# Performance work log

Measured on AMD Instinct MI355X. Metric: run time of the kernel, lower is better.

The kernel has to match this reference:

```python
import jax, jax.numpy as jnp
import numpy as np
import math

B, N, M, D, HID, OUT = 8, 2048, 2048, 1024, 1024, 1024

def setup_inputs() -> dict:
    key = jax.random.key(0)
    k1, k2, k3, k4, k5, k6 = jax.random.split(key, 6)
    h1 = jax.random.normal(k1, (B, N, D), dtype=jnp.float32)
    h2 = jax.random.normal(k2, (B, M, D), dtype=jnp.float32)
    mask = jax.random.randint(k3, (B, N, M), 0, 2, dtype=jnp.int32)
    # nn.Linear(in, out, bias=False) weight has shape (out, in)
    Wq = jax.random.normal(k4, (HID, D), dtype=jnp.float32) / math.sqrt(D)
    Wk = jax.random.normal(k5, (HID, D), dtype=jnp.float32) / math.sqrt(D)
    Wv = jax.random.normal(k6, (OUT, D), dtype=jnp.float32) / math.sqrt(D)
    return {"h1": h1, "h2": h2, "mask": mask, "Wq": Wq, "Wk": Wk, "Wv": Wv}

def reference(h1, h2, mask, Wq, Wk, Wv):
    Q = jnp.einsum('bnd,hd->bnh', h1, Wq)            # (B,N,HID)
    K = jnp.einsum('bmd,hd->bmh', h2, Wk)            # (B,M,HID)
    V = jnp.einsum('bmd,od->bmo', h2, Wv)            # (B,M,OUT)
    E = jnp.einsum('bnh,bmh->bnm', Q, K)             # (B,N,M) scores
    # NOTE: original masks E BEFORE dividing by sqrt(hidden_d)
    E = jnp.where(mask == 0, jnp.float32(-1e10), E)
    A = jax.nn.softmax(E / math.sqrt(HID), axis=2)
    return jnp.einsum('bnm,bmo->bno', A, V)          # (B,N,OUT)
```

## Files before the change

kernel.cpp:

```cpp
#include <hip/hip_runtime.h>


using f16   = _Float16;
using f16x4 = __attribute__((ext_vector_type(4))) _Float16;
using f16x8 = __attribute__((ext_vector_type(8))) _Float16;
using f32x4 = __attribute__((ext_vector_type(4))) float;

typedef unsigned int u32_g __attribute__((address_space(1)));
typedef unsigned int u32_l __attribute__((address_space(3)));

__device__ __forceinline__ void gl_lds16(const f16* g, f16* l) {
    __builtin_amdgcn_global_load_lds((const u32_g*)g, (u32_l*)l, 16, 0, 0);
}

template <int EPI, int GDEC, int LGX>
__global__ __launch_bounds__(256)
void gemm_nt_f16(const f16* __restrict__ A, const f16* __restrict__ B,
                 void* __restrict__ Cv, const int* __restrict__ Mask,
                 int N, int K, long sA, long sB, long sC, long sMask)
{
    int bx, by, bz;
    if constexpr (GDEC == 0) {
        bx = blockIdx.x; by = blockIdx.y; bz = blockIdx.z;
    } else {
        int l = blockIdx.x;
        bz = l & 7; bx = (l >> 3) & ((1 << LGX) - 1); by = l >> (3 + LGX);
    }
    const f16* Ab = A + (long)bz * sA;
    const f16* Bb = B + (long)bz * sB;
    const int bm0 = by * 128;
    const int bn0 = bx * 128;

    const int tid  = threadIdx.x;
    const int lane = tid & 63;
    const int wid  = tid >> 6;
    const int wm   = (wid >> 1) * 64;
    const int wn   = (wid & 1)  * 64;
    const int lr   = lane & 15;
    const int quad = lane >> 4;

    __shared__ f16 As[128 * 32];
    __shared__ f16 Bs[128 * 32];

    const int r0 = tid >> 2, b0 = tid & 3;
    const int r1 = r0 + 64;
    const int k0blk = (b0 ^ ((r0 >> 1) & 3)) << 3;
    const int k1blk = (b0 ^ ((r1 >> 1) & 3)) << 3;
    const f16* gA0 = Ab + (long)(bm0 + r0) * K + k0blk;
    const f16* gA1 = Ab + (long)(bm0 + r1) * K + k1blk;
    const f16* gB0 = Bb + (long)(bn0 + r0) * K + k0blk;
    const f16* gB1 = Bb + (long)(bn0 + r1) * K + k1blk;
    f16* lA0 = As + wid * 512;
    f16* lA1 = As + 2048 + wid * 512;
    f16* lB0 = Bs + wid * 512;
    f16* lB1 = Bs + 2048 + wid * 512;

    const int kb = ((quad ^ ((lr >> 1) & 3)) << 3);

    f32x4 acc[4][4] = {};
    f32x4 rs[4] = {};
    f16x8 bones;
#pragma unroll
    for (int j = 0; j < 8; ++j) bones[j] = (f16)1.0f;

    for (int k0 = 0; k0 < K; k0 += 32) {
        gl_lds16(gA0 + k0, lA0);
        gl_lds16(gA1 + k0, lA1);
        gl_lds16(gB0 + k0, lB0);
        gl_lds16(gB1 + k0, lB1);
        __syncthreads();

        f16x8 af[4], bfr[4];
#pragma unroll
        for (int i = 0; i < 4; ++i)
            af[i] = *(const f16x8*)(&As[(wm + i * 16 + lr) * 32 + kb]);
#pragma unroll
        for (int j = 0; j < 4; ++j)
            bfr[j] = *(const f16x8*)(&Bs[(wn + j * 16 + lr) * 32 + kb]);

        if constexpr (EPI == 2) {
#pragma unroll
            for (int i = 0; i < 4; ++i)
                rs[i] = __builtin_amdgcn_mfma_f32_16x16x32_f16(af[i], bones, rs[i], 0, 0, 0);
        }
#pragma unroll
        for (int i = 0; i < 4; ++i)
#pragma unroll
            for (int j = 0; j < 4; ++j)
                acc[i][j] = __builtin_amdgcn_mfma_f32_16x16x32_f16(af[i], bfr[j], acc[i][j], 0, 0, 0);
        __syncthreads();
    }

    if constexpr (EPI == 0) {
        f16* C = (f16*)Cv + (long)bz * sC;
#pragma unroll
        for (int i = 0; i < 4; ++i)
#pragma unroll
            for (int j = 0; j < 4; ++j)
#pragma unroll
                for (int r = 0; r < 4; ++r) {
                    long idx = (long)(bm0 + wm + i * 16 + quad * 4 + r) * N
                             + (bn0 + wn + j * 16 + lr);
                    C[idx] = (f16)acc[i][j][r];
                }
    } else if constexpr (EPI == 1) {
        f16* C = (f16*)Cv + (long)bz * sC;
        const int* Mk = Mask + (long)bz * sMask;
#pragma unroll
        for (int i = 0; i < 4; ++i)
#pragma unroll
            for (int j = 0; j < 4; ++j)
#pragma unroll
                for (int r = 0; r < 4; ++r) {
                    long idx = (long)(bm0 + wm + i * 16 + quad * 4 + r) * N
                             + (bn0 + wn + j * 16 + lr);
                    float v = (Mk[idx] == 0) ? -1e10f : acc[i][j][r];
                    C[idx] = (f16)__expf(v * 0.03125f);
                }
    } else {
        float* C = (float*)Cv + (long)bz * sC;
#pragma unroll
        for (int i = 0; i < 4; ++i) {
            float inv[4];
#pragma unroll
            for (int r = 0; r < 4; ++r) {
                float s = rs[i][r];
                inv[r] = (s > 0.f) ? 1.0f / s : 0.f;
            }
#pragma unroll
            for (int j = 0; j < 4; ++j)
#pragma unroll
                for (int r = 0; r < 4; ++r) {
                    long idx = (long)(bm0 + wm + i * 16 + quad * 4 + r) * N
                             + (bn0 + wn + j * 16 + lr);
                    C[idx] = acc[i][j][r] * inv[r];
                }
        }
    }
}

__global__ __launch_bounds__(256)
void cvt_f32_f16(const float* __restrict__ src, f16* __restrict__ dst)
{
    long i = ((long)blockIdx.x * 256 + threadIdx.x) * 4;
    float4 v = *(const float4*)(src + i);
    f16x4 o;
    o[0] = (f16)v.x; o[1] = (f16)v.y; o[2] = (f16)v.z; o[3] = (f16)v.w;
    *(f16x4*)(dst + i) = o;
}

__global__ __launch_bounds__(256)
void cvt_w3(const float* __restrict__ a, const float* __restrict__ b,
            const float* __restrict__ c,
            f16* __restrict__ oa, f16* __restrict__ ob, f16* __restrict__ oc)
{
    int bid = blockIdx.x;
    const float* s; f16* d;
    if (bid < 1024)      { s = a; d = oa; }
    else if (bid < 2048) { s = b; d = ob; bid -= 1024; }
    else                 { s = c; d = oc; bid -= 2048; }
    long i = ((long)bid * 256 + threadIdx.x) * 4;
    float4 v = *(const float4*)(s + i);
    f16x4 o;
    o[0] = (f16)v.x; o[1] = (f16)v.y; o[2] = (f16)v.z; o[3] = (f16)v.w;
    *(f16x4*)(d + i) = o;
}

extern "C" void kernel_launch(void* const* d_in, const int* in_sizes, int n_in,
                              void* d_out, int out_size, void* d_ws, size_t ws_size,
                              hipStream_t stream)
{
    const float* h1   = (const float*)d_in[0];
    const float* h2   = (const float*)d_in[1];
    const int*   mask = (const int*)d_in[2];
    const float* Wq   = (const float*)d_in[3];
    const float* Wk   = (const float*)d_in[4];
    const float* Wv   = (const float*)d_in[5];
    float* out = (float*)d_out;

    char* ws = (char*)d_ws;
    f16* h1f = (f16*)(ws);
    f16* h2f = (f16*)(ws + 33554432);
    f16* Wqf = (f16*)(ws + 67108864);
    f16* Wkf = (f16*)(ws + 69206016);
    f16* Wvf = (f16*)(ws + 71303168);
    f16* SP  = (f16*)(ws + 33554432);
    f16* Vt  = (f16*)(ws);
    f16* Qf  = (f16*)d_out;
    f16* Kp  = (f16*)((char*)d_out + 33554432);

    dim3 blk(256);

    cvt_f32_f16<<<dim3(16384), blk, 0, stream>>>(h1, h1f);
    cvt_f32_f16<<<dim3(16384), blk, 0, stream>>>(h2, h2f);
    cvt_w3<<<dim3(3072), blk, 0, stream>>>(Wq, Wk, Wv, Wqf, Wkf, Wvf);

    gemm_nt_f16<0, 0, 0><<<dim3(8, 128, 1), blk, 0, stream>>>(h1f, Wqf, Qf,
        nullptr, 1024, 1024, 0, 0, 0, 0);
    gemm_nt_f16<0, 0, 0><<<dim3(8, 128, 1), blk, 0, stream>>>(h2f, Wkf, Kp,
        nullptr, 1024, 1024, 0, 0, 0, 0);
    gemm_nt_f16<0, 0, 0><<<dim3(16, 8, 8), blk, 0, stream>>>(Wvf, h2f, Vt,
        nullptr, 2048, 1024, 0, (long)2048 * 1024, (long)1024 * 2048, 0);
    gemm_nt_f16<1, 1, 4><<<dim3(2048), blk, 0, stream>>>(Qf, Kp, SP,
        mask, 2048, 1024, (long)2048 * 1024, (long)2048 * 1024,
        (long)2048 * 2048, (long)2048 * 2048);
    gemm_nt_f16<2, 1, 3><<<dim3(1024), blk, 0, stream>>>(SP, Vt, out,
        nullptr, 1024, 2048, (long)2048 * 2048, (long)1024 * 2048,
        (long)2048 * 1024, 0);
}
```

Before: 686.5 us.

## Replace 128x128 GEMM with 256x256 tile, 4-stage LDS pipeline and 8 waves

Rewrites the shared NT GEMM to use 256x256 block tiles with 512 threads, each wave computing 128x64. K tiles are prefetched three tiles ahead into a 4-buffer LDS ring with async global-to-LDS loads and split-half barriers, and MFMA sections are raised to high priority. The goal is more data reuse per loaded tile and overlap of global loads with MFMA work, in place of the old load-sync-compute loop. In exchange it uses 128KB of LDS and much larger accumulator register sets, and the SV GEMM drops to only 256 blocks, which could underfill the GPU.

```diff
diff --git a/kernel.cpp b/kernel.cpp
--- a/kernel.cpp
+++ b/kernel.cpp
@@ -13,12 +13,87 @@
     __builtin_amdgcn_global_load_lds((const u32_g*)g, (u32_l*)l, 16, 0, 0);
 }
 
+#define FENCE() asm volatile("" ::: "memory")
+#define BAR()   do { FENCE(); __builtin_amdgcn_s_barrier(); FENCE(); } while (0)
+
+#define MFMA_HALF(A0_, A1_, A2_, A3_, RG_)                                               \
+  do {                                                                                   \
+    if constexpr (EPI == 2) {                                                            \
+      rs[RG_+0] = __builtin_amdgcn_mfma_f32_16x16x32_f16(A0_, bones, rs[RG_+0], 0,0,0);  \
+      rs[RG_+1] = __builtin_amdgcn_mfma_f32_16x16x32_f16(A1_, bones, rs[RG_+1], 0,0,0);  \
+      rs[RG_+2] = __builtin_amdgcn_mfma_f32_16x16x32_f16(A2_, bones, rs[RG_+2], 0,0,0);  \
+      rs[RG_+3] = __builtin_amdgcn_mfma_f32_16x16x32_f16(A3_, bones, rs[RG_+3], 0,0,0);  \
+    }                                                                                    \
+    acc[RG_+0][0] = __builtin_amdgcn_mfma_f32_16x16x32_f16(A0_, b0, acc[RG_+0][0],0,0,0);\
+    acc[RG_+0][1] = __builtin_amdgcn_mfma_f32_16x16x32_f16(A0_, b1, acc[RG_+0][1],0,0,0);\
+    acc[RG_+0][2] = __builtin_amdgcn_mfma_f32_16x16x32_f16(A0_, b2, acc[RG_+0][2],0,0,0);\
+    acc[RG_+0][3] = __builtin_amdgcn_mfma_f32_16x16x32_f16(A0_, b3, acc[RG_+0][3],0,0,0);\
+    acc[RG_+1][0] = __builtin_amdgcn_mfma_f32_16x16x32_f16(A1_, b0, acc[RG_+1][0],0,0,0);\
+    acc[RG_+1][1] = __builtin_amdgcn_mfma_f32_16x16x32_f16(A1_, b1, acc[RG_+1][1],0,0,0);\
+    acc[RG_+1][2] = __builtin_amdgcn_mfma_f32_16x16x32_f16(A1_, b2, acc[RG_+1][2],0,0,0);\
+    acc[RG_+1][3] = __builtin_amdgcn_mfma_f32_16x16x32_f16(A1_, b3, acc[RG_+1][3],0,0,0);\
+    acc[RG_+2][0] = __builtin_amdgcn_mfma_f32_16x16x32_f16(A2_, b0, acc[RG_+2][0],0,0,0);\
+    acc[RG_+2][1] = __builtin_amdgcn_mfma_f32_16x16x32_f16(A2_, b1, acc[RG_+2][1],0,0,0);\
+    acc[RG_+2][2] = __builtin_amdgcn_mfma_f32_16x16x32_f16(A2_, b2, acc[RG_+2][2],0,0,0);\
+    acc[RG_+2][3] = __builtin_amdgcn_mfma_f32_16x16x32_f16(A2_, b3, acc[RG_+2][3],0,0,0);\
+    acc[RG_+3][0] = __builtin_amdgcn_mfma_f32_16x16x32_f16(A3_, b0, acc[RG_+3][0],0,0,0);\
+    acc[RG_+3][1] = __builtin_amdgcn_mfma_f32_16x16x32_f16(A3_, b1, acc[RG_+3][1],0,0,0);\
+    acc[RG_+3][2] = __builtin_amdgcn_mfma_f32_16x16x32_f16(A3_, b2, acc[RG_+3][2],0,0,0);\
+    acc[RG_+3][3] = __builtin_amdgcn_mfma_f32_16x16x32_f16(A3_, b3, acc[RG_+3][3],0,0,0);\
+  } while (0)
+
+#define TILE_BODY(T_, STG_, VM_)                                                         \
+  {                                                                                      \
+    const f16* bufA_ = smem + ((T_) & 3) * 16384;                                        \
+    const f16* bufB_ = bufA_ + 8192;                                                     \
+    f16x8 a0_, a1_, a2_, a3_, b0, b1, b2, b3;                                            \
+    a0_ = *(const f16x8*)(bufA_ + offA);                                                 \
+    a1_ = *(const f16x8*)(bufA_ + offA + 512);                                           \
+    a2_ = *(const f16x8*)(bufA_ + offA + 1024);                                          \
+    a3_ = *(const f16x8*)(bufA_ + offA + 1536);                                          \
+    b0  = *(const f16x8*)(bufB_ + offB);                                                 \
+    b1  = *(const f16x8*)(bufB_ + offB + 512);                                           \
+    b2  = *(const f16x8*)(bufB_ + offB + 1024);                                          \
+    b3  = *(const f16x8*)(bufB_ + offB + 1536);                                          \
+    if (STG_) {                                                                          \
+      f16* dA_ = ldsAw + ((T_ + 3) & 3) * 16384;                                         \
+      const f16* gA_ = gAs + (long)(T_ + 3) * 32;                                        \
+      gl_lds16(gA_, dA_);                                                                \
+      gl_lds16(gA_ + sweep, dA_ + 4096);                                                 \
+    }                                                                                    \
+    BAR();                                                                               \
+    asm volatile("s_waitcnt lgkmcnt(0)" ::: "memory");                                   \
+    __builtin_amdgcn_s_setprio(1);                                                       \
+    MFMA_HALF(a0_, a1_, a2_, a3_, 0);                                                    \
+    __builtin_amdgcn_s_setprio(0);                                                       \
+    BAR();                                                                               \
+    a0_ = *(const f16x8*)(bufA_ + offA + 2048);                                          \
+    a1_ = *(const f16x8*)(bufA_ + offA + 2560);                                          \
+    a2_ = *(const f16x8*)(bufA_ + offA + 3072);                                          \
+    a3_ = *(const f16x8*)(bufA_ + offA + 3584);                                          \
+    if (STG_) {                                                                          \
+      f16* dB_ = ldsBw + ((T_ + 3) & 3) * 16384;                                         \
+      const f16* gB_ = gBs + (long)(T_ + 3) * 32;                                        \
+      gl_lds16(gB_, dB_);                                                                \
+      gl_lds16(gB_ + sweep, dB_ + 4096);                                                 \
+    }                                                                                    \
+    BAR();                                                                               \
+    asm volatile("s_waitcnt lgkmcnt(0)" ::: "memory");                                   \
+    __builtin_amdgcn_s_setprio(1);                                                       \
+    MFMA_HALF(a0_, a1_, a2_, a3_, 4);                                                    \
+    __builtin_amdgcn_s_setprio(0);                                                       \
+    asm volatile(VM_ ::: "memory");                                                      \
+    BAR();                                                                               \
+  }
+
 template <int EPI, int GDEC, int LGX>
-__global__ __launch_bounds__(256)
-void gemm_nt_f16(const f16* __restrict__ A, const f16* __restrict__ B,
-                 void* __restrict__ Cv, const int* __restrict__ Mask,
-                 int N, int K, long sA, long sB, long sC, long sMask)
-{
+__global__ __launch_bounds__(512, 2)
+void gemm256_nt_f16(const f16* __restrict__ A, const f16* __restrict__ B,
+                    void* __restrict__ Cv, const int* __restrict__ Mask,
+                    int N, int K, long sA, long sB, long sC, long sMask)
+{
+    __shared__ f16 smem[4 * 16384];
+
     int bx, by, bz;
     if constexpr (GDEC == 0) {
         bx = blockIdx.x; by = blockIdx.y; bz = blockIdx.z;
@@ -28,112 +103,103 @@
     }
     const f16* Ab = A + (long)bz * sA;
     const f16* Bb = B + (long)bz * sB;
-    const int bm0 = by * 128;
-    const int bn0 = bx * 128;
+    const int bm0 = by * 256;
+    const int bn0 = bx * 256;
 
     const int tid  = threadIdx.x;
     const int lane = tid & 63;
     const int wid  = tid >> 6;
-    const int wm   = (wid >> 1) * 64;
-    const int wn   = (wid & 1)  * 64;
+    const int wm   = (wid >> 2) * 128;
+    const int wn   = (wid & 3)  * 64;
     const int lr   = lane & 15;
     const int quad = lane >> 4;
-
-    __shared__ f16 As[128 * 32];
-    __shared__ f16 Bs[128 * 32];
-
-    const int r0 = tid >> 2, b0 = tid & 3;
-    const int r1 = r0 + 64;
-    const int k0blk = (b0 ^ ((r0 >> 1) & 3)) << 3;
-    const int k1blk = (b0 ^ ((r1 >> 1) & 3)) << 3;
-    const f16* gA0 = Ab + (long)(bm0 + r0) * K + k0blk;
-    const f16* gA1 = Ab + (long)(bm0 + r1) * K + k1blk;
-    const f16* gB0 = Bb + (long)(bn0 + r0) * K + k0blk;
-    const f16* gB1 = Bb + (long)(bn0 + r1) * K + k1blk;
-    f16* lA0 = As + wid * 512;
-    f16* lA1 = As + 2048 + wid * 512;
-    f16* lB0 = Bs + wid * 512;
-    f16* lB1 = Bs + 2048 + wid * 512;
-
-    const int kb = ((quad ^ ((lr >> 1) & 3)) << 3);
-
-    f32x4 acc[4][4] = {};
-    f32x4 rs[4] = {};
+    const int kb   = (quad ^ ((lr >> 1) & 3)) << 3;
+
+    const int offA = (wm + lr) * 32 + kb;
+    const int offB = (wn + lr) * 32 + kb;
+
+    const int r0 = tid >> 2, c0 = tid & 3;
+    const int sw = (c0 ^ ((r0 >> 1) & 3)) << 3;
+    const f16* gAs = Ab + (long)(bm0 + r0) * K + sw;
+    const f16* gBs = Bb + (long)(bn0 + r0) * K + sw;
+    const long sweep = (long)128 * K;
+
+    f16* ldsAw = smem + wid * 512;
+    f16* ldsBw = smem + 8192 + wid * 512;
+
+    f32x4 acc[8][4] = {};
+    f32x4 rs[8] = {};
     f16x8 bones;
 #pragma unroll
     for (int j = 0; j < 8; ++j) bones[j] = (f16)1.0f;
 
-    for (int k0 = 0; k0 < K; k0 += 32) {
-        gl_lds16(gA0 + k0, lA0);
-        gl_lds16(gA1 + k0, lA1);
-        gl_lds16(gB0 + k0, lB0);
-        gl_lds16(gB1 + k0, lB1);
-        __syncthreads();
-
-        f16x8 af[4], bfr[4];
-#pragma unroll
-        for (int i = 0; i < 4; ++i)
-            af[i] = *(const f16x8*)(&As[(wm + i * 16 + lr) * 32 + kb]);
-#pragma unroll
-        for (int j = 0; j < 4; ++j)
-            bfr[j] = *(const f16x8*)(&Bs[(wn + j * 16 + lr) * 32 + kb]);
-
-        if constexpr (EPI == 2) {
-#pragma unroll
-            for (int i = 0; i < 4; ++i)
-                rs[i] = __builtin_amdgcn_mfma_f32_16x16x32_f16(af[i], bones, rs[i], 0, 0, 0);
-        }
-#pragma unroll
-        for (int i = 0; i < 4; ++i)
-#pragma unroll
-            for (int j = 0; j < 4; ++j)
-                acc[i][j] = __builtin_amdgcn_mfma_f32_16x16x32_f16(af[i], bfr[j], acc[i][j], 0, 0, 0);
-        __syncthreads();
-    }
+    const int nt = K >> 5;
+
+#pragma unroll
+    for (int tt = 0; tt < 3; ++tt) {
+        const f16* gA = gAs + (long)tt * 32;
+        const f16* gB = gBs + (long)tt * 32;
+        f16* dA = ldsAw + tt * 16384;
+        f16* dB = ldsBw + tt * 16384;
+        gl_lds16(gA, dA);
+        gl_lds16(gA + sweep, dA + 4096);
+        gl_lds16(gB, dB);
+        gl_lds16(gB + sweep, dB + 4096);
+    }
+    asm volatile("s_waitcnt vmcnt(8)" ::: "memory");
+    BAR();
+
+#pragma unroll 1
+    for (int t = 0; t < nt - 3; ++t) {
+        TILE_BODY(t, 1, "s_waitcnt vmcnt(8)");
+    }
+    TILE_BODY(nt - 3, 0, "s_waitcnt vmcnt(4)");
+    TILE_BODY(nt - 2, 0, "s_waitcnt vmcnt(0)");
+    TILE_BODY(nt - 1, 0, "");
 
     if constexpr (EPI == 0) {
         f16* C = (f16*)Cv + (long)bz * sC;
 #pragma unroll
-        for (int i = 0; i < 4; ++i)
-#pragma unroll
-            for (int j = 0; j < 4; ++j)
+        for (int rg = 0; rg < 8; ++rg)
+#pragma unroll
+            for (int cg = 0; cg < 4; ++cg)
 #pragma unroll
                 for (int r = 0; r < 4; ++r) {
-                    long idx = (long)(bm0 + wm + i * 16 + quad * 4 + r) * N
-                             + (bn0 + wn + j * 16 + lr);
-                    C[idx] = (f16)acc[i][j][r];
+                    long idx = (long)(bm0 + wm + rg * 16 + quad * 4 + r) * N
+                             + (bn0 + wn + cg * 16 + lr);
+                    C[idx] = (f16)acc[rg][cg][r];
                 }
     } else if constexpr (EPI == 1) {
         f16* C = (f16*)Cv + (long)bz * sC;
         const int* Mk = Mask + (long)bz * sMask;
 #pragma unroll
-        for (int i = 0; i < 4; ++i)
-#pragma unroll
-            for (int j = 0; j < 4; ++j)
+        for (int rg = 0; rg < 8; ++rg)
+#pragma unroll
+            for (int cg = 0; cg < 4; ++cg)
 #pragma unroll
                 for (int r = 0; r < 4; ++r) {
-                    long idx = (long)(bm0 + wm + i * 16 + quad * 4 + r) * N
-                             + (bn0 + wn + j * 16 + lr);
-                    float v = (Mk[idx] == 0) ? -1e10f : acc[i][j][r];
+                    long idx = (long)(bm0 + wm + rg * 16 + quad * 4 + r) * N
+                             + (bn0 + wn + cg * 16 + lr);
+                    float v = (Mk[idx] == 0) ? -1e10f : acc[rg][cg][r];
                     C[idx] = (f16)__expf(v * 0.03125f);
                 }
     } else {
         float* C = (float*)Cv + (long)bz * sC;
 #pragma unroll
-        for (int i = 0; i < 4; ++i) {
+        for (int rg = 0; rg < 8; ++rg) {
             float inv[4];
 #pragma unroll
             for (int r = 0; r < 4; ++r) {
-                float s = rs[i][r];
+                float s = rs[rg][r];
                 inv[r] = (s > 0.f) ? 1.0f / s : 0.f;
             }
 #pragma unroll
-            for (int j = 0; j < 4; ++j)
+            for (int cg = 0; cg < 4; ++cg)
 #pragma unroll
                 for (int r = 0; r < 4; ++r) {
-                    long idx = (long)(bm0 + wm + i * 16 + quad * 4 + r) * N
-                             + (bn0 + wn + j * 16 + lr);
-                    C[idx] = acc[i][j][r] * inv[r];
+                    long idx = (long)(bm0 + wm + rg * 16 + quad * 4 + r) * N
+                             + (bn0 + wn + cg * 16 + lr);
+                    C[idx] = acc[rg][cg][r] * inv[r];
                 }
         }
     }
@@ -190,21 +256,22 @@
     f16* Kp  = (f16*)((char*)d_out + 33554432);
 
     dim3 blk(256);
+    dim3 blk5(512);
 
     cvt_f32_f16<<<dim3(16384), blk, 0, stream>>>(h1, h1f);
     cvt_f32_f16<<<dim3(16384), blk, 0, stream>>>(h2, h2f);
     cvt_w3<<<dim3(3072), blk, 0, stream>>>(Wq, Wk, Wv, Wqf, Wkf, Wvf);
 
-    gemm_nt_f16<0, 0, 0><<<dim3(8, 128, 1), blk, 0, stream>>>(h1f, Wqf, Qf,
+    gemm256_nt_f16<0, 0, 0><<<dim3(4, 64, 1), blk5, 0, stream>>>(h1f, Wqf, Qf,
         nullptr, 1024, 1024, 0, 0, 0, 0);
-    gemm_nt_f16<0, 0, 0><<<dim3(8, 128, 1), blk, 0, stream>>>(h2f, Wkf, Kp,
+    gemm256_nt_f16<0, 0, 0><<<dim3(4, 64, 1), blk5, 0, stream>>>(h2f, Wkf, Kp,
         nullptr, 1024, 1024, 0, 0, 0, 0);
-    gemm_nt_f16<0, 0, 0><<<dim3(16, 8, 8), blk, 0, stream>>>(Wvf, h2f, Vt,
+    gemm256_nt_f16<0, 0, 0><<<dim3(8, 4, 8), blk5, 0, stream>>>(Wvf, h2f, Vt,
         nullptr, 2048, 1024, 0, (long)2048 * 1024, (long)1024 * 2048, 0);
-    gemm_nt_f16<1, 1, 4><<<dim3(2048), blk, 0, stream>>>(Qf, Kp, SP,
+    gemm256_nt_f16<1, 1, 3><<<dim3(512), blk5, 0, stream>>>(Qf, Kp, SP,
         mask, 2048, 1024, (long)2048 * 1024, (long)2048 * 1024,
         (long)2048 * 2048, (long)2048 * 2048);
-    gemm_nt_f16<2, 1, 3><<<dim3(1024), blk, 0, stream>>>(SP, Vt, out,
+    gemm256_nt_f16<2, 1, 2><<<dim3(256), blk5, 0, stream>>>(SP, Vt, out,
         nullptr, 1024, 2048, (long)2048 * 2048, (long)1024 * 2048,
         (long)2048 * 1024, 0);
 }
```

New measurement: 555.7 us. 1.24x faster.
